# Performance work log

Measured on AMD Instinct MI355X. Metric: run time of the kernel, lower is better.

Reference implementation:

```python
import jax, jax.numpy as jnp
import numpy as np

L, D = 8192, 1024


def binary_operator_diag(q_i, q_j):
    # elementwise (diagonal) linear-recurrence combine: h_j = A_j * h_i + b_j
    A_i, b_i = q_i
    A_j, b_j = q_j
    return A_j * A_i, A_j * b_i + b_j


def setup_inputs() -> dict:
    key = jax.random.key(0)
    k_in, k_u, k_th, k_bre, k_bim = jax.random.split(key, 5)
    inputs = jax.random.normal(k_in, (L, D), dtype=jnp.float32)
    # stable LRU init: |lambda| = exp(-exp(nu)) = sqrt(u), u in (0.01, 0.99)
    u = jax.random.uniform(k_u, (D,), jnp.float32, 0.01, 0.99)
    nu = jnp.log(-0.5 * jnp.log(u))
    # phase stored in log-space (forward uses exp(theta))
    theta = jnp.log(jax.random.uniform(k_th, (D,), jnp.float32, 1e-3, 6.28))
    gamma_log = 0.5 * jnp.log(1.0 - u)  # = log(sqrt(1 - |lambda|^2))
    norm = np.float32(np.sqrt(2.0 * D))
    B_re = jax.random.normal(k_bre, (D, D), jnp.float32) / norm
    B_im = jax.random.normal(k_bim, (D, D), jnp.float32) / norm
    return {"inputs": inputs, "theta": theta, "nu": nu,
            "gamma_log": gamma_log, "B_re": B_re, "B_im": B_im}


def reference(inputs, theta, nu, gamma_log, B_re, B_im):
    # diagonal transition: lambda = exp(-exp(nu) + i*exp(theta)), shape [D]
    diag_lambda = jnp.exp(-jnp.exp(nu) + 1j * jnp.exp(theta))
    # normalized input matrix: (B_re + i B_im) * exp(gamma_log)[:, None]
    B_norm = (B_re + 1j * B_im) * jnp.exp(gamma_log)[:, None]  # [D, D] complex
    # Bu[t] = B_norm @ u_t  -> batched as one GEMM: [L, D] complex
    Bu = jnp.einsum('ld,kd->lk', inputs.astype(B_norm.dtype), B_norm)
    Lambda_elements = jnp.broadcast_to(diag_lambda[None, :], Bu.shape)
    # parallel associative scan over time (axis 0), elementwise over channels
    _, hidden_states = jax.lax.associative_scan(
        binary_operator_diag, (Lambda_elements, Bu))
    return hidden_states.real + inputs
```

## Files before the change

kernel.cpp:

```cpp
#include <hip/hip_runtime.h>
#include <cstdint>
#include <cstddef>

typedef float  f32x4  __attribute__((ext_vector_type(4)));
typedef short  bf16x8 __attribute__((ext_vector_type(8)));
typedef unsigned short u16x8 __attribute__((ext_vector_type(8)));

#define L_SEQ   8192
#define D_DIM   1024
#define N_COL   2048
#define N_PAIR  512
#define CHUNK_T 16
#define N_CHUNK 512

__device__ __forceinline__ unsigned short f2bf(float f) {
  unsigned int b = __float_as_uint(f);
  b += 0x7FFFu + ((b >> 16) & 1u);
  return (unsigned short)(b >> 16);
}
__device__ __forceinline__ float bf2f(unsigned short u) {
  return __uint_as_float((unsigned int)u << 16);
}
__device__ __forceinline__ void gload_lds16(const void* g, void* lds) {
  __builtin_amdgcn_global_load_lds(
      (const __attribute__((address_space(1))) void*)g,
      (__attribute__((address_space(3))) void*)lds, 16, 0, 0);
}
__device__ __forceinline__ float2 cmul(float2 a, float2 b) {
  return make_float2(a.x * b.x - a.y * b.y, a.x * b.y + a.y * b.x);
}
__device__ __forceinline__ float2 csqr(float2 a) {
  return make_float2(a.x * a.x - a.y * a.y, 2.f * a.x * a.y);
}
__device__ __forceinline__ void cfma2(const float4& lm, float2& h0, float2& h1,
                                      const float4& v) {
  float nr0 = fmaf(lm.x, h0.x, fmaf(-lm.y, h0.y, v.x));
  float ni0 = fmaf(lm.x, h0.y, fmaf(lm.y, h0.x, v.y));
  float nr1 = fmaf(lm.z, h1.x, fmaf(-lm.w, h1.y, v.z));
  float ni1 = fmaf(lm.z, h1.y, fmaf(lm.w, h1.x, v.w));
  h0.x = nr0; h0.y = ni0; h1.x = nr1; h1.y = ni1;
}

__global__ __launch_bounds__(256) void k_prep(
    const float* __restrict__ in, const float* __restrict__ Bre,
    const float* __restrict__ Bim, const float* __restrict__ gamma_log,
    const float* __restrict__ theta, const float* __restrict__ nu,
    unsigned short* __restrict__ A, unsigned short* __restrict__ W,
    float2* __restrict__ lam) {
  int b = blockIdx.x;
  if (b < 4096) {
    int i = b * 256 + threadIdx.x;
    const float4* p = (const float4*)in;
    float4 a = p[2 * i], c = p[2 * i + 1];
    u16x8 o;
    o[0] = f2bf(a.x); o[1] = f2bf(a.y); o[2] = f2bf(a.z); o[3] = f2bf(a.w);
    o[4] = f2bf(c.x); o[5] = f2bf(c.y); o[6] = f2bf(c.z); o[7] = f2bf(c.w);
    *(u16x8*)(A + (size_t)i * 8) = o;
  } else if (b < 5120) {
    int t = (b - 4096) * 256 + threadIdx.x;
    int row = t >> 7;
    int seg = t & 127;
    int k = row >> 1;
    const float* src = (row & 1) ? Bim : Bre;
    float g = expf(gamma_log[k]);
    const float4* p = (const float4*)(src + (size_t)k * D_DIM + seg * 8);
    float4 a = p[0], c = p[1];
    u16x8 o;
    o[0] = f2bf(a.x * g); o[1] = f2bf(a.y * g); o[2] = f2bf(a.z * g); o[3] = f2bf(a.w * g);
    o[4] = f2bf(c.x * g); o[5] = f2bf(c.y * g); o[6] = f2bf(c.z * g); o[7] = f2bf(c.w * g);
    *(u16x8*)(W + (size_t)row * D_DIM + seg * 8) = o;
  } else {
    int k = (b - 5120) * 256 + threadIdx.x;
    if (k < D_DIM) {
      float mod = expf(-expf(nu[k]));
      float ang = expf(theta[k]);
      lam[k] = make_float2(mod * cosf(ang), mod * sinf(ang));
    }
  }
}

__global__ __launch_bounds__(512, 1) void k_gemm(const unsigned short* __restrict__ A,
                                                 const unsigned short* __restrict__ W,
                                                 unsigned short* __restrict__ Bu16,
                                                 float2* __restrict__ agg2,
                                                 const float2* __restrict__ lam) {
  extern __shared__ char smem[];

  const int tid = threadIdx.x;
  const int l = tid & 63, w = tid >> 6;
  const int wm = w >> 2, wn = w & 3;

  int orig = blockIdx.x;
  int wgid = (orig & 7) * 32 + (orig >> 3);
  const int mt = wgid >> 3, nt = wgid & 7;
  const size_t m0 = (size_t)mt * 256, n0 = (size_t)nt * 256;

  const int srow = tid >> 3;
  const int scs  = tid & 7;
  const int cA   = scs ^ (srow & 7);
  const size_t srcoff0 = (size_t)srow * 2048 + (size_t)cA * 16;
  const size_t srcoff1 = srcoff0 + 64 * 2048;
  const int dst0 = tid * 16, dst1 = 8192 + tid * 16;

#define STAGE(Mptr, Mbase, Msel, bb, hh, TT) do {                                   \
    const char* s_ = (const char*)(Mptr) +                                          \
        (((Mbase) + (size_t)(hh) * 128) * 2048 + (size_t)(TT) * 128);               \
    char* d_ = smem + (Msel) * 65536 + (bb) * 32768 + (hh) * 16384;                 \
    gload_lds16(s_ + srcoff0, d_ + dst0);                                           \
    gload_lds16(s_ + srcoff1, d_ + dst1);                                           \
  } while (0)

  int aroff[8], broff[4];
#pragma unroll
  for (int fr = 0; fr < 8; ++fr) {
    int lrow = fr * 32 + wm * 16 + (l & 15);
    aroff[fr] = (lrow >> 7) * 16384 + (lrow & 127) * 128;
  }
#pragma unroll
  for (int fn = 0; fn < 4; ++fn) {
    int lrow = fn * 64 + wn * 16 + (l & 15);
    broff[fn] = (lrow >> 7) * 16384 + (lrow & 127) * 128;
  }
  const int swk0 = (((l >> 4)) ^ (l & 7)) << 4;
  const int swk1 = ((4 + (l >> 4)) ^ (l & 7)) << 4;

  f32x4 acc[8][4];
#pragma unroll
  for (int m = 0; m < 8; ++m)
#pragma unroll
    for (int n = 0; n < 4; ++n) acc[m][n] = (f32x4){0.f, 0.f, 0.f, 0.f};

  bf16x8 af[4][2], bfr[4][2];

#define LGKMC0 asm volatile("s_waitcnt lgkmcnt(0)" ::: "memory")
#define VMCNT4 asm volatile("s_waitcnt vmcnt(4)" ::: "memory")
#define VMCNT0 asm volatile("s_waitcnt vmcnt(0)" ::: "memory")
#define BAR()  do { asm volatile("" ::: "memory"); __builtin_amdgcn_s_barrier(); \
                    asm volatile("" ::: "memory"); } while (0)

  STAGE(W, n0, 1, 0, 0, 0);
  STAGE(A, m0, 0, 0, 1, 0);
  STAGE(A, m0, 0, 0, 0, 0);
  STAGE(W, n0, 1, 0, 1, 0);
  STAGE(W, n0, 1, 1, 0, 1);
  STAGE(A, m0, 0, 1, 1, 1);
  VMCNT4;
  BAR();

  for (int kt = 0; kt < 16; ++kt) {
    const int buf = kt & 1;
    const int abase = buf * 32768;
    const int bbase = 65536 + buf * 32768;
    const int b1 = (kt + 1) & 1, b2 = kt & 1;
    const bool s1 = (kt + 1 < 16), s2 = (kt + 2 < 16);

#pragma unroll
    for (int i = 0; i < 4; ++i) {
      af[i][0] = *(const bf16x8*)(smem + abase + aroff[i] + swk0);
      af[i][1] = *(const bf16x8*)(smem + abase + aroff[i] + swk1);
    }
#pragma unroll
    for (int fn = 0; fn < 2; ++fn) {
      bfr[fn][0] = *(const bf16x8*)(smem + bbase + broff[fn] + swk0);
      bfr[fn][1] = *(const bf16x8*)(smem + bbase + broff[fn] + swk1);
    }
    if (s1) STAGE(A, m0, 0, b1, 0, kt + 1);
    __builtin_amdgcn_s_setprio(1);
#pragma unroll
    for (int i = 0; i < 4; ++i)
#pragma unroll
      for (int fn = 0; fn < 2; ++fn) {
        acc[i][fn] = __builtin_amdgcn_mfma_f32_16x16x32_bf16(af[i][0], bfr[fn][0], acc[i][fn], 0, 0, 0);
        acc[i][fn] = __builtin_amdgcn_mfma_f32_16x16x32_bf16(af[i][1], bfr[fn][1], acc[i][fn], 0, 0, 0);
      }
    __builtin_amdgcn_s_setprio(0);
    LGKMC0;
    BAR();

#pragma unroll
    for (int fn = 2; fn < 4; ++fn) {
      bfr[fn][0] = *(const bf16x8*)(smem + bbase + broff[fn] + swk0);
      bfr[fn][1] = *(const bf16x8*)(smem + bbase + broff[fn] + swk1);
    }
    if (s1) STAGE(W, n0, 1, b1, 1, kt + 1);
    __builtin_amdgcn_s_setprio(1);
#pragma unroll
    for (int i = 0; i < 4; ++i)
#pragma unroll
      for (int fn = 2; fn < 4; ++fn) {
        acc[i][fn] = __builtin_amdgcn_mfma_f32_16x16x32_bf16(af[i][0], bfr[fn][0], acc[i][fn], 0, 0, 0);
        acc[i][fn] = __builtin_amdgcn_mfma_f32_16x16x32_bf16(af[i][1], bfr[fn][1], acc[i][fn], 0, 0, 0);
      }
    __builtin_amdgcn_s_setprio(0);
    LGKMC0;
    BAR();

#pragma unroll
    for (int i = 0; i < 4; ++i) {
      af[i][0] = *(const bf16x8*)(smem + abase + aroff[4 + i] + swk0);
      af[i][1] = *(const bf16x8*)(smem + abase + aroff[4 + i] + swk1);
    }
    if (s2) STAGE(W, n0, 1, b2, 0, kt + 2);
    __builtin_amdgcn_s_setprio(1);
#pragma unroll
    for (int i = 0; i < 4; ++i)
#pragma unroll
      for (int fn = 2; fn < 4; ++fn) {
        acc[4 + i][fn] = __builtin_amdgcn_mfma_f32_16x16x32_bf16(af[i][0], bfr[fn][0], acc[4 + i][fn], 0, 0, 0);
        acc[4 + i][fn] = __builtin_amdgcn_mfma_f32_16x16x32_bf16(af[i][1], bfr[fn][1], acc[4 + i][fn], 0, 0, 0);
      }
    __builtin_amdgcn_s_setprio(0);
    LGKMC0;
    BAR();

    if (s2) STAGE(A, m0, 0, b2, 1, kt + 2);
    __builtin_amdgcn_s_setprio(1);
#pragma unroll
    for (int i = 0; i < 4; ++i)
#pragma unroll
      for (int fn = 0; fn < 2; ++fn) {
        acc[4 + i][fn] = __builtin_amdgcn_mfma_f32_16x16x32_bf16(af[i][0], bfr[fn][0], acc[4 + i][fn], 0, 0, 0);
        acc[4 + i][fn] = __builtin_amdgcn_mfma_f32_16x16x32_bf16(af[i][1], bfr[fn][1], acc[4 + i][fn], 0, 0, 0);
      }
    __builtin_amdgcn_s_setprio(0);
    if (kt < 14) VMCNT4; else VMCNT0;
    BAR();
  }
#undef STAGE

#pragma unroll
  for (int fr = 0; fr < 8; ++fr)
#pragma unroll
    for (int fn = 0; fn < 4; ++fn) {
      int col = fn * 64 + wn * 16 + (l & 15);
#pragma unroll
      for (int j = 0; j < 4; ++j) {
        int row = fr * 32 + wm * 16 + (l >> 4) * 4 + j;
        int byte = row * 512 + ((col * 2) ^ ((row & 7) << 4));
        *(unsigned short*)(smem + byte) = f2bf(acc[fr][fn][j]);
      }
    }
  __syncthreads();

  {
    unsigned short* gbase = Bu16 + m0 * N_COL + n0;
#pragma unroll
    for (int pass = 0; pass < 16; ++pass) {
      int row = pass * 16 + (tid >> 5);
      int c = tid & 31;
      int byte = row * 512 + ((c * 16) ^ ((row & 7) << 4));
      f32x4 v = *(const f32x4*)(smem + byte);
      *(f32x4*)(gbase + (size_t)row * N_COL + c * 8) = v;
    }
  }

#pragma unroll
  for (int i = 0; i < 4; ++i) {
    int q = i * 512 + tid;
    int c = q >> 7, ch = q & 127;
    float2 lmv = lam[(n0 >> 1) + ch];
    float2 h = {0.f, 0.f};
#pragma unroll
    for (int s = 0; s < 16; ++s) {
      int row = c * 16 + s;
      int byte = row * 512 + ((ch * 4) ^ ((row & 7) << 4));
      unsigned int pr = *(const unsigned int*)(smem + byte);
      float br = bf2f((unsigned short)(pr & 0xFFFFu));
      float bi = bf2f((unsigned short)(pr >> 16));
      float nr = fmaf(lmv.x, h.x, fmaf(-lmv.y, h.y, br));
      float ni = fmaf(lmv.x, h.y, fmaf(lmv.y, h.x, bi));
      h.x = nr; h.y = ni;
    }
    agg2[(size_t)(mt * 16 + c) * 1024 + (n0 >> 1) + ch] = h;
  }
}

__global__ __launch_bounds__(256) void k_scan2(const float4* __restrict__ agg4,
                                               const float4* __restrict__ lam4,
                                               float4* __restrict__ carry4) {
  int wave = blockIdx.x * 4 + (threadIdx.x >> 6);
  int lane = threadIdx.x & 63;
  int j = wave;
  float4 lm = lam4[j];
  float2 lT0 = {lm.x, lm.y}, lT1 = {lm.z, lm.w};
#pragma unroll
  for (int i = 0; i < 4; ++i) { lT0 = csqr(lT0); lT1 = csqr(lT1); }

  float4 a[8];
  float2 T0 = {0.f, 0.f}, T1 = {0.f, 0.f};
  float4 lTv = make_float4(lT0.x, lT0.y, lT1.x, lT1.y);
#pragma unroll
  for (int i = 0; i < 8; ++i) {
    a[i] = agg4[(size_t)(lane * 8 + i) * N_PAIR + j];
    cfma2(lTv, T0, T1, a[i]);
  }

  float2 M0 = lT0, M1 = lT1;
#pragma unroll
  for (int i = 0; i < 3; ++i) { M0 = csqr(M0); M1 = csqr(M1); }
  float2 S0 = T0, S1 = T1;
#pragma unroll
  for (int d = 1; d < 64; d <<= 1) {
    float2 u0, u1;
    u0.x = __shfl_up(S0.x, d); u0.y = __shfl_up(S0.y, d);
    u1.x = __shfl_up(S1.x, d); u1.y = __shfl_up(S1.y, d);
    if (lane >= d) {
      float2 m0 = cmul(M0, u0), m1 = cmul(M1, u1);
      S0.x += m0.x; S0.y += m0.y; S1.x += m1.x; S1.y += m1.y;
    }
    M0 = csqr(M0); M1 = csqr(M1);
  }
  float2 P0, P1;
  P0.x = __shfl_up(S0.x, 1); P0.y = __shfl_up(S0.y, 1);
  P1.x = __shfl_up(S1.x, 1); P1.y = __shfl_up(S1.y, 1);
  if (lane == 0) { P0 = make_float2(0.f, 0.f); P1 = make_float2(0.f, 0.f); }

#pragma unroll
  for (int i = 0; i < 8; ++i) {
    carry4[(size_t)(lane * 8 + i) * N_PAIR + j] = make_float4(P0.x, P0.y, P1.x, P1.y);
    cfma2(lTv, P0, P1, a[i]);
  }
}

__global__ __launch_bounds__(256) void k_scan3(const u16x8* __restrict__ Bu8,
                                               const float4* __restrict__ lam4,
                                               const float4* __restrict__ carry4,
                                               const ushort4* __restrict__ inA,
                                               float4* __restrict__ out4) {
  int t = blockIdx.x * 256 + threadIdx.x;
  int c = t >> 8, q = t & 255;
  float4 lm0 = lam4[2 * q], lm1 = lam4[2 * q + 1];
  float4 cv0 = carry4[(size_t)c * N_PAIR + 2 * q];
  float4 cv1 = carry4[(size_t)c * N_PAIR + 2 * q + 1];
  float2 h0 = {cv0.x, cv0.y}, h1 = {cv0.z, cv0.w};
  float2 h2 = {cv1.x, cv1.y}, h3 = {cv1.z, cv1.w};
#pragma unroll
  for (int s = 0; s < CHUNK_T; ++s) {
    size_t row = (size_t)c * CHUNK_T + s;
    u16x8 b = Bu8[row * 256 + q];
    float4 v0 = make_float4(bf2f(b[0]), bf2f(b[1]), bf2f(b[2]), bf2f(b[3]));
    float4 v1 = make_float4(bf2f(b[4]), bf2f(b[5]), bf2f(b[6]), bf2f(b[7]));
    cfma2(lm0, h0, h1, v0);
    cfma2(lm1, h2, h3, v1);
    ushort4 iv = inA[row * 256 + q];
    out4[row * 256 + q] = make_float4(h0.x + bf2f(iv.x), h1.x + bf2f(iv.y),
                                      h2.x + bf2f(iv.z), h3.x + bf2f(iv.w));
  }
}

extern "C" void kernel_launch(void* const* d_in, const int* in_sizes, int n_in,
                              void* d_out, int out_size, void* d_ws, size_t ws_size,
                              hipStream_t stream) {
  (void)in_sizes; (void)n_in; (void)out_size; (void)ws_size;
  const float* inputs    = (const float*)d_in[0];
  const float* theta     = (const float*)d_in[1];
  const float* nu        = (const float*)d_in[2];
  const float* gamma_log = (const float*)d_in[3];
  const float* Bre       = (const float*)d_in[4];
  const float* Bim       = (const float*)d_in[5];

  char* ws = (char*)d_ws;
  float2*         lam   = (float2*)ws;
  unsigned short* A     = (unsigned short*)(ws + (1 << 16));
  unsigned short* W     = (unsigned short*)(ws + (1 << 16) + (16u << 20));
  unsigned short* Bu16  = (unsigned short*)(ws + (1 << 16) + (20u << 20));
  float2*         agg   = (float2*)(ws + (1 << 16) + (52u << 20));
  float4*         carry = (float4*)(ws + (1 << 16) + (56u << 20));

  hipFuncSetAttribute((const void*)k_gemm,
                      hipFuncAttributeMaxDynamicSharedMemorySize, 131072);

  k_prep<<<5124, 256, 0, stream>>>(inputs, Bre, Bim, gamma_log, theta, nu, A, W, lam);
  k_gemm<<<256, 512, 131072, stream>>>(A, W, Bu16, agg, (const float2*)lam);
  k_scan2<<<N_PAIR / 4, 256, 0, stream>>>((const float4*)agg, (const float4*)lam, carry);
  k_scan3<<<(N_CHUNK * 256) / 256, 256, 0, stream>>>((const u16x8*)Bu16,
                                                     (const float4*)lam, carry,
                                                     (const ushort4*)A,
                                                     (float4*)d_out);
}
```

Baseline: 69.59 us.

## Switch GEMM to 32x32x16 MFMA tiles and batch LDS loads in chunk scan

Replaces the 16x16x32 bf16 MFMA fragment layout with 32x32x16 MFMA, changing per-wave tile ownership (each wave now covers contiguous 128x64 regions), the LDS fragment offsets, the swizzle indices and the epilogue row mapping. Larger MFMA tiles reduce LDS fragment reads per FLOP and the instruction count. The chunk-local scan epilogue also loads all 16 LDS values up front before the serial recurrence, to overlap LDS latency. Risks include higher register pressure from 16-wide accumulators and new LDS bank-conflict patterns.

```diff
diff --git a/kernel.cpp b/kernel.cpp
--- a/kernel.cpp
+++ b/kernel.cpp
@@ -2,8 +2,9 @@
 #include <cstdint>
 #include <cstddef>
 
-typedef float  f32x4  __attribute__((ext_vector_type(4)));
-typedef short  bf16x8 __attribute__((ext_vector_type(8)));
+typedef float  f32x4   __attribute__((ext_vector_type(4)));
+typedef float  f32x16  __attribute__((ext_vector_type(16)));
+typedef short  bf16x8  __attribute__((ext_vector_type(8)));
 typedef unsigned short u16x8 __attribute__((ext_vector_type(8)));
 
 #define L_SEQ   8192
@@ -110,27 +111,31 @@
     gload_lds16(s_ + srcoff1, d_ + dst1);                                           \
   } while (0)
 
-  int aroff[8], broff[4];
-#pragma unroll
-  for (int fr = 0; fr < 8; ++fr) {
-    int lrow = fr * 32 + wm * 16 + (l & 15);
-    aroff[fr] = (lrow >> 7) * 16384 + (lrow & 127) * 128;
-  }
-#pragma unroll
-  for (int fn = 0; fn < 4; ++fn) {
-    int lrow = fn * 64 + wn * 16 + (l & 15);
-    broff[fn] = (lrow >> 7) * 16384 + (lrow & 127) * 128;
-  }
-  const int swk0 = (((l >> 4)) ^ (l & 7)) << 4;
-  const int swk1 = ((4 + (l >> 4)) ^ (l & 7)) << 4;
-
-  f32x4 acc[8][4];
-#pragma unroll
-  for (int m = 0; m < 8; ++m)
-#pragma unroll
-    for (int n = 0; n < 4; ++n) acc[m][n] = (f32x4){0.f, 0.f, 0.f, 0.f};
-
-  bf16x8 af[4][2], bfr[4][2];
+  int aroff[4], broff[2];
+#pragma unroll
+  for (int mb = 0; mb < 4; ++mb) {
+    int lrow = wm * 128 + mb * 32 + (l & 31);
+    aroff[mb] = (lrow >> 7) * 16384 + (lrow & 127) * 128;
+  }
+#pragma unroll
+  for (int nb = 0; nb < 2; ++nb) {
+    int lrow = wn * 64 + nb * 32 + (l & 31);
+    broff[nb] = (lrow >> 7) * 16384 + (lrow & 127) * 128;
+  }
+  int swk[4];
+#pragma unroll
+  for (int ks = 0; ks < 4; ++ks)
+    swk[ks] = ((ks * 2 + (l >> 5)) ^ (l & 7)) << 4;
+
+  f32x16 acc[4][2];
+#pragma unroll
+  for (int mb = 0; mb < 4; ++mb)
+#pragma unroll
+    for (int nb = 0; nb < 2; ++nb)
+#pragma unroll
+      for (int r = 0; r < 16; ++r) acc[mb][nb][r] = 0.f;
+
+  bf16x8 af[2][4], bfr[2][4];
 
 #define LGKMC0 asm volatile("s_waitcnt lgkmcnt(0)" ::: "memory")
 #define VMCNT4 asm volatile("s_waitcnt vmcnt(4)" ::: "memory")
@@ -155,60 +160,53 @@
     const bool s1 = (kt + 1 < 16), s2 = (kt + 2 < 16);
 
 #pragma unroll
-    for (int i = 0; i < 4; ++i) {
-      af[i][0] = *(const bf16x8*)(smem + abase + aroff[i] + swk0);
-      af[i][1] = *(const bf16x8*)(smem + abase + aroff[i] + swk1);
-    }
-#pragma unroll
-    for (int fn = 0; fn < 2; ++fn) {
-      bfr[fn][0] = *(const bf16x8*)(smem + bbase + broff[fn] + swk0);
-      bfr[fn][1] = *(const bf16x8*)(smem + bbase + broff[fn] + swk1);
-    }
+    for (int mb = 0; mb < 2; ++mb)
+#pragma unroll
+      for (int ks = 0; ks < 4; ++ks)
+        af[mb][ks] = *(const bf16x8*)(smem + abase + aroff[mb] + swk[ks]);
+#pragma unroll
+    for (int ks = 0; ks < 4; ++ks)
+      bfr[0][ks] = *(const bf16x8*)(smem + bbase + broff[0] + swk[ks]);
     if (s1) STAGE(A, m0, 0, b1, 0, kt + 1);
     __builtin_amdgcn_s_setprio(1);
 #pragma unroll
-    for (int i = 0; i < 4; ++i)
-#pragma unroll
-      for (int fn = 0; fn < 2; ++fn) {
-        acc[i][fn] = __builtin_amdgcn_mfma_f32_16x16x32_bf16(af[i][0], bfr[fn][0], acc[i][fn], 0, 0, 0);
-        acc[i][fn] = __builtin_amdgcn_mfma_f32_16x16x32_bf16(af[i][1], bfr[fn][1], acc[i][fn], 0, 0, 0);
-      }
+    for (int mb = 0; mb < 2; ++mb)
+#pragma unroll
+      for (int ks = 0; ks < 4; ++ks)
+        acc[mb][0] = __builtin_amdgcn_mfma_f32_32x32x16_bf16(af[mb][ks], bfr[0][ks],
+                                                             acc[mb][0], 0, 0, 0);
     __builtin_amdgcn_s_setprio(0);
     LGKMC0;
     BAR();
 
 #pragma unroll
-    for (int fn = 2; fn < 4; ++fn) {
-      bfr[fn][0] = *(const bf16x8*)(smem + bbase + broff[fn] + swk0);
-      bfr[fn][1] = *(const bf16x8*)(smem + bbase + broff[fn] + swk1);
-    }
+    for (int ks = 0; ks < 4; ++ks)
+      bfr[1][ks] = *(const bf16x8*)(smem + bbase + broff[1] + swk[ks]);
     if (s1) STAGE(W, n0, 1, b1, 1, kt + 1);
     __builtin_amdgcn_s_setprio(1);
 #pragma unroll
-    for (int i = 0; i < 4; ++i)
-#pragma unroll
-      for (int fn = 2; fn < 4; ++fn) {
-        acc[i][fn] = __builtin_amdgcn_mfma_f32_16x16x32_bf16(af[i][0], bfr[fn][0], acc[i][fn], 0, 0, 0);
-        acc[i][fn] = __builtin_amdgcn_mfma_f32_16x16x32_bf16(af[i][1], bfr[fn][1], acc[i][fn], 0, 0, 0);
-      }
+    for (int mb = 0; mb < 2; ++mb)
+#pragma unroll
+      for (int ks = 0; ks < 4; ++ks)
+        acc[mb][1] = __builtin_amdgcn_mfma_f32_32x32x16_bf16(af[mb][ks], bfr[1][ks],
+                                                             acc[mb][1], 0, 0, 0);
     __builtin_amdgcn_s_setprio(0);
     LGKMC0;
     BAR();
 
 #pragma unroll
-    for (int i = 0; i < 4; ++i) {
-      af[i][0] = *(const bf16x8*)(smem + abase + aroff[4 + i] + swk0);
-      af[i][1] = *(const bf16x8*)(smem + abase + aroff[4 + i] + swk1);
-    }
+    for (int mb = 0; mb < 2; ++mb)
+#pragma unroll
+      for (int ks = 0; ks < 4; ++ks)
+        af[mb][ks] = *(const bf16x8*)(smem + abase + aroff[2 + mb] + swk[ks]);
     if (s2) STAGE(W, n0, 1, b2, 0, kt + 2);
     __builtin_amdgcn_s_setprio(1);
 #pragma unroll
-    for (int i = 0; i < 4; ++i)
-#pragma unroll
-      for (int fn = 2; fn < 4; ++fn) {
-        acc[4 + i][fn] = __builtin_amdgcn_mfma_f32_16x16x32_bf16(af[i][0], bfr[fn][0], acc[4 + i][fn], 0, 0, 0);
-        acc[4 + i][fn] = __builtin_amdgcn_mfma_f32_16x16x32_bf16(af[i][1], bfr[fn][1], acc[4 + i][fn], 0, 0, 0);
-      }
+    for (int mb = 0; mb < 2; ++mb)
+#pragma unroll
+      for (int ks = 0; ks < 4; ++ks)
+        acc[2 + mb][1] = __builtin_amdgcn_mfma_f32_32x32x16_bf16(af[mb][ks], bfr[1][ks],
+                                                                 acc[2 + mb][1], 0, 0, 0);
     __builtin_amdgcn_s_setprio(0);
     LGKMC0;
     BAR();
@@ -216,12 +214,11 @@
     if (s2) STAGE(A, m0, 0, b2, 1, kt + 2);
     __builtin_amdgcn_s_setprio(1);
 #pragma unroll
-    for (int i = 0; i < 4; ++i)
-#pragma unroll
-      for (int fn = 0; fn < 2; ++fn) {
-        acc[4 + i][fn] = __builtin_amdgcn_mfma_f32_16x16x32_bf16(af[i][0], bfr[fn][0], acc[4 + i][fn], 0, 0, 0);
-        acc[4 + i][fn] = __builtin_amdgcn_mfma_f32_16x16x32_bf16(af[i][1], bfr[fn][1], acc[4 + i][fn], 0, 0, 0);
-      }
+    for (int mb = 0; mb < 2; ++mb)
+#pragma unroll
+      for (int ks = 0; ks < 4; ++ks)
+        acc[2 + mb][0] = __builtin_amdgcn_mfma_f32_32x32x16_bf16(af[mb][ks], bfr[0][ks],
+                                                                 acc[2 + mb][0], 0, 0, 0);
     __builtin_amdgcn_s_setprio(0);
     if (kt < 14) VMCNT4; else VMCNT0;
     BAR();
@@ -229,15 +226,15 @@
 #undef STAGE
 
 #pragma unroll
-  for (int fr = 0; fr < 8; ++fr)
-#pragma unroll
-    for (int fn = 0; fn < 4; ++fn) {
-      int col = fn * 64 + wn * 16 + (l & 15);
-#pragma unroll
-      for (int j = 0; j < 4; ++j) {
-        int row = fr * 32 + wm * 16 + (l >> 4) * 4 + j;
+  for (int mb = 0; mb < 4; ++mb)
+#pragma unroll
+    for (int nb = 0; nb < 2; ++nb) {
+      int col = wn * 64 + nb * 32 + (l & 31);
+#pragma unroll
+      for (int r = 0; r < 16; ++r) {
+        int row = wm * 128 + mb * 32 + (r & 3) + 8 * (r >> 2) + 4 * (l >> 5);
         int byte = row * 512 + ((col * 2) ^ ((row & 7) << 4));
-        *(unsigned short*)(smem + byte) = f2bf(acc[fr][fn][j]);
+        *(unsigned short*)(smem + byte) = f2bf(acc[mb][nb][r]);
       }
     }
   __syncthreads();
@@ -259,14 +256,17 @@
     int q = i * 512 + tid;
     int c = q >> 7, ch = q & 127;
     float2 lmv = lam[(n0 >> 1) + ch];
-    float2 h = {0.f, 0.f};
+    unsigned int pr[16];
 #pragma unroll
     for (int s = 0; s < 16; ++s) {
       int row = c * 16 + s;
-      int byte = row * 512 + ((ch * 4) ^ ((row & 7) << 4));
-      unsigned int pr = *(const unsigned int*)(smem + byte);
-      float br = bf2f((unsigned short)(pr & 0xFFFFu));
-      float bi = bf2f((unsigned short)(pr >> 16));
+      pr[s] = *(const unsigned int*)(smem + row * 512 + ((ch * 4) ^ ((row & 7) << 4)));
+    }
+    float2 h = {0.f, 0.f};
+#pragma unroll
+    for (int s = 0; s < 16; ++s) {
+      float br = bf2f((unsigned short)(pr[s] & 0xFFFFu));
+      float bi = bf2f((unsigned short)(pr[s] >> 16));
       float nr = fmaf(lmv.x, h.x, fmaf(-lmv.y, h.y, br));
       float ni = fmaf(lmv.x, h.y, fmaf(lmv.y, h.x, bi));
       h.x = nr; h.y = ni;
```

After: 74.23 us. 1.07x slower.
